# Kernel tuning notes

Hardware: AMD Instinct MI355X
Metric: run time of the kernel (lower is better)

The kernel has to match this reference:

```python
import jax, jax.numpy as jnp
import numpy as np

LATENT_SHAPES = [(192, 2, 2), (48, 4, 4), (24, 8, 8), (12, 16, 16), (6, 32, 32)]
B = 4          # batch
M = 32         # num_bases
HT, WT = 32, 32  # target spatial size = spatial size of z[-1] = (H/2, W/2)
EPS = 1e-3
CT = sum(s[0] for s in LATENT_SHAPES)  # 282


def _forward_fft(zs):
    # strided zero-insertion upsample of each latent to (HT, WT), concat channels, 2D FFT
    ups = []
    for zi in zs:
        b, c, h, w = zi.shape
        rh, rw = HT // h, WT // w
        u = jnp.zeros((b, c, HT, WT), zi.dtype).at[..., ::rh, ::rw].set(zi)
        ups.append(u)
    z = jnp.concatenate(ups, axis=1)            # (B, CT, HT, WT)
    return jnp.fft.fftn(z, axes=(-2, -1))       # complex64


def _inverse_fft(v_fft):
    # inverse FFT, take real part, split channels per level, strided downsample
    v = jnp.fft.ifftn(v_fft, axes=(-2, -1)).real  # (B, M, CT, HT, WT)
    splits = np.cumsum([s[0] for s in LATENT_SHAPES])[:-1]
    parts = jnp.split(v, splits, axis=-3)
    out = []
    for vi, (c, h, w) in zip(parts, LATENT_SHAPES):
        rh, rw = HT // h, WT // w
        out.append(vi[..., ::rh, ::rw])           # (B, M, c, h, w)
    return out


def _vector_field(zs, L, lam):
    z_fft = _forward_fft(zs)
    La = (L - jnp.swapaxes(L, -1, -2)).astype(jnp.complex64)        # antisymmetric (M, CT, CT)
    lam_a = (lam - jnp.roll(jnp.flip(lam, (1, 2)), (1, 1), axis=(1, 2))) * 1j  # (M, HT, WT) imaginary
    v_fft = jnp.einsum('mcd,bchw->bmdhw', La, z_fft)                 # (B, M, CT, HT, WT) complex
    v_fft = v_fft * lam_a[None, :, None, :, :]
    return _inverse_fft(v_fft)


def _log_prob(ws, zs, L, lam):
    S_ww = sum(jnp.einsum('bchw,bchw->b', wi, wi) for wi in ws)      # (B,)
    v = _vector_field(zs, L, lam)
    S_zz = sum(jnp.einsum('bnchw,bmchw->bnm', vi, vi) for vi in v)   # (B, M, M)
    S_zw = sum(jnp.einsum('bnchw,bchw->bn', vi, wi) for vi, wi in zip(v, ws))  # (B, M)
    var = jnp.maximum(jnp.mean(jnp.diagonal(S_zz, axis1=-2, axis2=-1), -1), 1e-6)
    std = jnp.sqrt(var)
    S_zz = S_zz / var[:, None, None]
    S_zw = S_zw / std[:, None]
    I = jnp.eye(M, dtype=S_zz.dtype)
    Mm = S_zz + EPS * I
    trace = EPS * S_ww + jnp.einsum('bn,bn->b', S_zw, S_zw)
    Lh = jnp.linalg.cholesky(Mm)
    logdet = 2.0 * jnp.sum(jnp.log(jnp.diagonal(Lh, axis1=-2, axis2=-1)), -1)
    return 0.5 * (logdet - trace)


def setup_inputs() -> dict:
    key = jax.random.key(0)
    ks = jax.random.split(key, 12)
    inp = {}
    for i, (c, h, w) in enumerate(LATENT_SHAPES):
        inp[f'z{i}'] = jax.random.normal(ks[i], (B, c, h, w), jnp.float32)
        inp[f'w{i}'] = jax.random.normal(ks[5 + i], (B, c, h, w), jnp.float32)
    inp['L'] = jax.random.normal(ks[10], (M, CT, CT), jnp.float32) * np.float32(1.0 / np.sqrt(CT))
    inp['lam'] = jax.random.normal(ks[11], (M, HT, WT), jnp.float32)
    return inp


def reference(z0, z1, z2, z3, z4, w0, w1, w2, w3, w4, L, lam):
    return _log_prob([w0, w1, w2, w3, w4], [z0, z1, z2, z3, z4], L, lam)
```

## Files before the change

kernel.cpp:

```cpp
#include <hip/hip_runtime.h>
#include <math.h>

#define NB 4
#define NM 32
#define CTOT 282
#define EPSV 1e-3f

__constant__ int g_cL[5]   = {192,48,24,12,6};
__constant__ int g_hL[5]   = {2,4,8,16,32};
__constant__ int g_coff[5] = {0,192,240,264,276};
__constant__ int g_zo[5]   = {0,768,1536,3072,6144};
__constant__ int g_po[4]   = {0,4,20,84};

__constant__ int t_lo[48] = {0,0,0,0,0,0,0,0,0,0,0,0,0,0,0,0,
                             0,0,0,0,0,0,0,0,0,0,0,0,0,0,0,0,
                             1,1,1,1,1,1,1,1, 2,2,2,2, 3,3, 4,4};
__constant__ int t_d0[48] = {0,6,12,18,24,30,36,42,48,54,60,66,72,78,84,90,
                             96,102,108,114,120,126,132,138,144,150,156,162,168,174,180,186,
                             192,198,204,210,216,222,228,234, 240,246,252,258, 264,270, 276,279};
__constant__ int t_nd[48] = {6,6,6,6,6,6,6,6,6,6,6,6,6,6,6,6,
                             6,6,6,6,6,6,6,6,6,6,6,6,6,6,6,6,
                             6,6,6,6,6,6,6,6, 6,6,6,6, 6,6, 3,3};

__constant__ int dft_l[30]  = {0,0,0, 1,1,1, 2,2,2,2,2,2,
                               3,3,3,3,3,3,3,3,3,3,3,3, 4,4,4,4,4,4};
__constant__ int dft_c0[30] = {0,64,128, 0,16,32, 0,4,8,12,16,20,
                               0,1,2,3,4,5,6,7,8,9,10,11, 0,1,2,3,4,5};
__constant__ int dft_nc[30] = {64,64,64, 16,16,16, 4,4,4,4,4,4,
                               1,1,1,1,1,1,1,1,1,1,1,1, 1,1,1,1,1,1};

#define N_LA     (NM*CTOT*CTOT)
#define OFF_LAT  0
#define OFF_ZRE  (OFF_LAT + N_LA)
#define OFF_ZIM  (OFF_ZRE + NB*12288)
#define OFF_WRE  (OFF_ZIM + NB*12288)
#define OFF_WIM  (OFF_WRE + NB*12288)
#define OFF_LAM  (OFF_WIM + NB*12288)
#define OFF_LAMF (OFF_LAM + NM*1024)
#define OFF_UR   (OFF_LAMF + NM*340)
#define OFF_UI   (OFF_UR + NB*NM*6*340)
#define OFF_VRE  (OFF_UI + NB*NM*6*340)
#define OFF_VIM  (OFF_VRE + NB*NM*12288)
#define OFF_SZZ  (OFF_VIM + NB*NM*12288)
#define OFF_SZW  (OFF_SZZ + NB*NM*NM)
#define OFF_SWW  (OFF_SZW + NB*NM)

#define PRE_LAT   (NM*81)
#define PRE_LAMF  (PRE_LAT + NM)
#define PRE_DFT   (PRE_LAMF + 2*NB*30)
#define PRE_SWW   (PRE_DFT + NB)
#define PRE_ZERO  (PRE_SWW + 17)

__global__ void __launch_bounds__(256) k_pre(
    const float* z0,const float* z1,const float* z2,const float* z3,const float* z4,
    const float* w0,const float* w1,const float* w2,const float* w3,const float* w4,
    const float* __restrict__ L, const float* __restrict__ lam, float* __restrict__ ws){
  __shared__ float shm[3136];
  int bid = blockIdx.x, t = threadIdx.x;
  if (bid < PRE_LAT){
    float* A  = shm;
    float* Bt = shm + 1056;
    int m = bid/81; int tl = bid%81;
    int d0 = (tl/9)*32, c0 = (tl%9)*32;
    const float* Lm = L + (size_t)m*CTOT*CTOT;
    for (int i=t;i<1024;i+=256){
      int r=i>>5, c=i&31;
      A[r*33+c]  = (c0+r<CTOT && d0+c<CTOT) ? Lm[(c0+r)*CTOT + d0+c] : 0.f;
      Bt[r*33+c] = (d0+r<CTOT && c0+c<CTOT) ? Lm[(d0+r)*CTOT + c0+c] : 0.f;
    }
    __syncthreads();
    float* out = ws + OFF_LAT + (size_t)m*CTOT*CTOT;
    for (int i=t;i<1024;i+=256){
      int r=i>>5, c=i&31;
      if (d0+r<CTOT && c0+c<CTOT)
        out[(size_t)(d0+r)*CTOT + c0+c] = A[c*33+r] - Bt[r*33+c];
    }
    return;
  }
  if (bid < PRE_LAMF){
    float* sA = shm;
    float* f3 = shm + 1024;
    float* f2 = shm + 1280;
    float* f1 = shm + 1344;
    int m = bid - PRE_LAT;
    for (int k=t;k<1024;k+=256){
      int ky=k>>5, kx=k&31;
      int nk = (((32-ky)&31)<<5) | ((32-kx)&31);
      float v = lam[(m<<10)+k] - lam[(m<<10)+nk];
      sA[k]=v;
      ws[OFF_LAM+(m<<10)+k]=v;
    }
    __syncthreads();
    { int s=t; int ky=s>>4, kx=s&15;
      float v = sA[(ky<<5)+kx]+sA[((ky+16)<<5)+kx]+sA[(ky<<5)+kx+16]+sA[((ky+16)<<5)+kx+16];
      f3[s]=v; ws[OFF_LAMF+m*340+84+s]=v; }
    __syncthreads();
    if (t<64){ int ky=t>>3, kx=t&7;
      float v = f3[(ky<<4)+kx]+f3[((ky+8)<<4)+kx]+f3[(ky<<4)+kx+8]+f3[((ky+8)<<4)+kx+8];
      f2[t]=v; ws[OFF_LAMF+m*340+20+t]=v; }
    __syncthreads();
    if (t<16){ int ky=t>>2, kx=t&3;
      float v = f2[(ky<<3)+kx]+f2[((ky+4)<<3)+kx]+f2[(ky<<3)+kx+4]+f2[((ky+4)<<3)+kx+4];
      f1[t]=v; ws[OFF_LAMF+m*340+4+t]=v; }
    __syncthreads();
    if (t<4){ int ky=t>>1, kx=t&1;
      float v = f1[(ky<<2)+kx]+f1[((ky+2)<<2)+kx]+f1[(ky<<2)+kx+2]+f1[((ky+2)<<2)+kx+2];
      ws[OFF_LAMF+m*340+t]=v; }
    return;
  }
  if (bid < PRE_DFT){
    float* sIn = shm;
    float* s1r = shm + 1024;
    float* s1i = shm + 2048;
    float* lc  = shm + 3072;
    float* lsn = shm + 3104;
    int i0 = bid - PRE_LAMF;
    int which = i0 / (NB*30);
    int rem = i0 % (NB*30);
    int b = rem / 30, j = rem % 30;
    int l = dft_l[j], c0 = dft_c0[j], nc = dft_nc[j];
    int h = g_hL[l], n = h*h;
    int elems = nc*n;
    const float* src;
    switch (which*5 + l){
      case 0: src=z0; break; case 1: src=z1; break; case 2: src=z2; break;
      case 3: src=z3; break; case 4: src=z4; break;
      case 5: src=w0; break; case 6: src=w1; break; case 7: src=w2; break;
      case 8: src=w3; break; default: src=w4; break;
    }
    for (int i=t;i<elems;i+=256) sIn[i] = src[(b*g_cL[l] + c0)*n + i];
    if (t<h){
      float ang = -6.2831853071795864f * (float)t / (float)h;
      lc[t] = cosf(ang); lsn[t] = sinf(ang);
    }
    __syncthreads();
    for (int p=t;p<elems;p+=256){
      int p2=p%n, cc=p/n;
      int y=p2/h, kx=p2-y*h;
      float re=0.f, im=0.f;
      for (int x=0;x<h;x++){
        int id = (kx*x)%h;
        float v = sIn[cc*n + y*h + x];
        re += v*lc[id]; im += v*lsn[id];
      }
      s1r[p]=re; s1i[p]=im;
    }
    __syncthreads();
    float scale = which ? 1.0f/(float)h : 1.0f;
    float* outR = ws + (which?OFF_WRE:OFF_ZRE) + b*12288 + g_zo[l] + c0*n;
    float* outI = ws + (which?OFF_WIM:OFF_ZIM) + b*12288 + g_zo[l] + c0*n;
    for (int p=t;p<elems;p+=256){
      int p2=p%n, cc=p/n;
      int ky=p2/h, kx=p2-(p2/h)*h;
      float re=0.f, im=0.f;
      for (int y=0;y<h;y++){
        int id=(ky*y)%h;
        float c=lc[id], s=lsn[id];
        float ar=s1r[cc*n + y*h + kx], ai=s1i[cc*n + y*h + kx];
        re += ar*c - ai*s;
        im += ar*s + ai*c;
      }
      outR[p]=re*scale; outI[p]=im*scale;
    }
    return;
  }
  if (bid < PRE_SWW){
    float* red = shm;
    int b = bid - PRE_DFT;
    const float* ptr[5] = {w0,w1,w2,w3,w4};
    float s = 0.f;
    for (int l=0;l<5;l++){
      int sz = g_cL[l]*g_hL[l]*g_hL[l];
      const float* p = ptr[l] + b*sz;
      for (int i=t;i<sz;i+=256){ float v=p[i]; s += v*v; }
    }
    red[t]=s; __syncthreads();
    for (int o=128;o>0;o>>=1){ if (t<o) red[t]+=red[t+o]; __syncthreads(); }
    if (t==0) ws[OFF_SWW + b] = red[0];
    return;
  }
  int i = (bid - PRE_SWW)*256 + t;
  if (i < NB*NM*NM + NB*NM) ws[OFF_SZZ + i] = 0.f;
}

__global__ void k_u(float* __restrict__ ws){
  __shared__ float pr[1024], pi[1024], q3r[256],q3i[256],q2r[64],q2i[64],q1r[16],q1i[16];
  int bid = blockIdx.x, t = threadIdx.x;
  int c = bid%6; int m = (bid/6)%NM; int b = bid/(6*NM);
  const float* la = ws+OFF_LAM+(m<<10);
  const float* zr = ws+OFF_ZRE+b*12288+6144+(c<<10);
  const float* zi = ws+OFF_ZIM+b*12288+6144+(c<<10);
  for (int k=t;k<1024;k+=256){ float f=la[k]; pr[k]=f*zr[k]; pi[k]=f*zi[k]; }
  __syncthreads();
  size_t base = (size_t)((b*NM+m)*6+c)*340;
  float* UR = ws+OFF_UR+base; float* UI = ws+OFF_UI+base;
  { int s=t; int ky=s>>4, kx=s&15;
    float r = pr[(ky<<5)+kx]+pr[((ky+16)<<5)+kx]+pr[(ky<<5)+kx+16]+pr[((ky+16)<<5)+kx+16];
    float ii= pi[(ky<<5)+kx]+pi[((ky+16)<<5)+kx]+pi[(ky<<5)+kx+16]+pi[((ky+16)<<5)+kx+16];
    q3r[s]=r; q3i[s]=ii; UR[84+s]=r; UI[84+s]=ii; }
  __syncthreads();
  if (t<64){ int ky=t>>3, kx=t&7;
    float r = q3r[(ky<<4)+kx]+q3r[((ky+8)<<4)+kx]+q3r[(ky<<4)+kx+8]+q3r[((ky+8)<<4)+kx+8];
    float ii= q3i[(ky<<4)+kx]+q3i[((ky+8)<<4)+kx]+q3i[(ky<<4)+kx+8]+q3i[((ky+8)<<4)+kx+8];
    q2r[t]=r; q2i[t]=ii; UR[20+t]=r; UI[20+t]=ii; }
  __syncthreads();
  if (t<16){ int ky=t>>2, kx=t&3;
    float r = q2r[(ky<<3)+kx]+q2r[((ky+4)<<3)+kx]+q2r[(ky<<3)+kx+4]+q2r[((ky+4)<<3)+kx+4];
    float ii= q2i[(ky<<3)+kx]+q2i[((ky+4)<<3)+kx]+q2i[(ky<<3)+kx+4]+q2i[((ky+4)<<3)+kx+4];
    q1r[t]=r; q1i[t]=ii; UR[4+t]=r; UI[4+t]=ii; }
  __syncthreads();
  if (t<4){ int ky=t>>1, kx=t&1;
    float r = q1r[(ky<<2)+kx]+q1r[((ky+2)<<2)+kx]+q1r[(ky<<2)+kx+2]+q1r[((ky+2)<<2)+kx+2];
    float ii= q1i[(ky<<2)+kx]+q1i[((ky+2)<<2)+kx]+q1i[(ky<<2)+kx+2]+q1i[((ky+2)<<2)+kx+2];
    UR[t]=r; UI[t]=ii; }
}

__global__ void __launch_bounds__(256) k_fold(float* __restrict__ ws){
  __shared__ float smem[9232];
  float* pre   = smem;
  float* pim   = smem + 2040;
  float* partr = smem + 4080;
  float* parti = smem + 5616;
  float* sLa   = smem + 7152;
  float* c64r  = smem + 7152;
  float* c64i  = smem + 7536;
  float* c16r  = smem + 7920;
  float* c16i  = smem + 8016;
  float* c4r   = smem + 8112;
  float* c4i   = smem + 8136;
  float* lamf  = smem + 8856;
  float* ssla  = smem + 9196;

  int t = threadIdx.x, bid = blockIdx.x;
  int m    = bid / (NB*48);
  int rem  = bid % (NB*48);
  int b    = rem / 48;
  int tile = rem % 48;
  int lo = t_lo[tile], d0 = t_d0[tile], nd = t_nd[tile];
  int ho = g_hL[lo];
  int nbins = ho*ho;
  const float* zreb = ws + OFF_ZRE + b*12288;
  const float* zimb = ws + OFF_ZIM + b*12288;
  const float* latm = ws + OFF_LAT + (size_t)m*CTOT*CTOT;

  for (int i=t;i<340;i+=256) lamf[i] = ws[OFF_LAMF + m*340 + i];
  for (int i=t;i<nd*282;i+=256){ int d=i/282, c=i-d*282; sLa[d*284+c] = latm[(size_t)(d0+d)*CTOT + c]; }
  if (t<nd*6){ int d=t/6, c=t-d*6; ssla[t] = latm[(size_t)(d0+d)*CTOT + 276 + c]; }

  int lA, kkA, c0A, nA;
  if (t<64){ lA=0; kkA=t&3; c0A=(t>>2)*12; nA=4; }
  else if (t<128){ int i=t-64; lA=1; kkA=i&15; c0A=(i>>4)*12; nA=16; }
  else { int i=t-128; lA=2; kkA=i&63; c0A=(i>>6)*12; nA=64; }
  float zAr[12], zAi[12], zBr[12], zBi[12];
  {
    const float* zr = zreb + g_zo[lA] + kkA;
    const float* zi = zimb + g_zo[lA] + kkA;
    #pragma unroll
    for (int c=0;c<12;c++){ zAr[c]=zr[(c0A+c)*nA]; zAi[c]=zi[(c0A+c)*nA]; }
    const float* zr3 = zreb + 3072 + t;
    const float* zi3 = zimb + 3072 + t;
    #pragma unroll
    for (int c=0;c<12;c++){ zBr[c]=zr3[c*256]; zBi[c]=zi3[c*256]; }
  }
  __syncthreads();

  int offA = g_coff[lA] + c0A;
  for (int d=0; d<nd; d++){
    const float4* laA = (const float4*)(sLa + d*284 + offA);
    const float4* laB = (const float4*)(sLa + d*284 + 264);
    float4 a0=laA[0], a1=laA[1], a2=laA[2];
    float4 b0=laB[0], b1=laB[1], b2=laB[2];
    float av[12] = {a0.x,a0.y,a0.z,a0.w, a1.x,a1.y,a1.z,a1.w, a2.x,a2.y,a2.z,a2.w};
    float bv[12] = {b0.x,b0.y,b0.z,b0.w, b1.x,b1.y,b1.z,b1.w, b2.x,b2.y,b2.z,b2.w};
    float prA=0.f, piA=0.f, prB=0.f, piB=0.f;
    #pragma unroll
    for (int c=0;c<12;c++){ prA+=av[c]*zAr[c]; piA+=av[c]*zAi[c]; }
    #pragma unroll
    for (int c=0;c<12;c++){ prB+=bv[c]*zBr[c]; piB+=bv[c]*zBi[c]; }
    partr[(d<<8)+t]=prA; parti[(d<<8)+t]=piA;
    pre[d*340+84+t]=prB; pim[d*340+84+t]=piB;
  }
  __syncthreads();

  for (int idx=t; idx<nd*84; idx+=256){
    int d=idx/84, s=idx-d*84;
    int base=d<<8;
    float r=0.f, ii=0.f;
    if (s<4){ for (int ch=0;ch<16;ch++){ int p=base+((ch<<2)|s); r+=partr[p]; ii+=parti[p]; } }
    else if (s<20){ int kk=s-4; for (int ch=0;ch<4;ch++){ int p=base+64+((ch<<4)|kk); r+=partr[p]; ii+=parti[p]; } }
    else { int kk=s-20; for (int ch=0;ch<2;ch++){ int p=base+128+((ch<<6)|kk); r+=partr[p]; ii+=parti[p]; } }
    pre[d*340+s]=r; pim[d*340+s]=ii;
  }
  __syncthreads();

  float sc = (float)ho/1024.f;
  if (lo==4){
    int dlb = d0 - 276;
    const float* lamA = ws + OFF_LAM + (m<<10);
    float* vRb = ws + OFF_VRE + (size_t)(b*NM+m)*12288 + 6144 + (dlb<<10);
    float* vIb = ws + OFF_VIM + (size_t)(b*NM+m)*12288 + 6144 + (dlb<<10);
    const float* z4r = zreb + 6144;
    const float* z4i = zimb + 6144;
    for (int q=t; q<1024; q+=256){
      int ky=q>>5, kx=q&31;
      int a0=((ky&1)<<1)|(kx&1);
      int a1=4+(((ky&3)<<2)|(kx&3));
      int a2=20+(((ky&7)<<3)|(kx&7));
      int a3=84+(((ky&15)<<4)|(kx&15));
      float zr_[6], zi_[6];
      #pragma unroll
      for (int c=0;c<6;c++){ zr_[c]=z4r[(c<<10)+q]; zi_[c]=z4i[(c<<10)+q]; }
      float lm = lamA[q]*sc;
      for (int d=0; d<nd; d++){
        const float* pd = pre + d*340; const float* qd = pim + d*340;
        float Br = pd[a0]+pd[a1]+pd[a2]+pd[a3];
        float Bi = qd[a0]+qd[a1]+qd[a2]+qd[a3];
        #pragma unroll
        for (int c=0;c<6;c++){ float a=ssla[d*6+c]; Br+=a*zr_[c]; Bi+=a*zi_[c]; }
        vRb[(d<<10)+q] = -lm*Bi;
        vIb[(d<<10)+q] =  lm*Br;
      }
    }
    return;
  }

  if (lo<3){
    for (int idx=t; idx<nd*64; idx+=256){
      int d=idx>>6, k2=idx&63, ky=k2>>3, kx=k2&7;
      const float* pd = pre + d*340 + 84; const float* qd = pim + d*340 + 84;
      float r=0.f, ii=0.f;
      #pragma unroll
      for (int jy=0;jy<2;jy++)
        #pragma unroll
        for (int jx=0;jx<2;jx++){
          int a = ((ky+8*jy)<<4) | (kx+8*jx);
          float f = lamf[84+a];
          r += f*pd[a]; ii += f*qd[a];
        }
      if (lo<2){ float f=lamf[20+k2]; r+=f*pre[d*340+20+k2]; ii+=f*pim[d*340+20+k2]; }
      c64r[idx]=r; c64i[idx]=ii;
    }
  }
  {
    const float* URg = ws + OFF_UR + (size_t)((b*NM+m)*6)*340 + g_po[lo];
    const float* UIg = ws + OFF_UI + (size_t)((b*NM+m)*6)*340 + g_po[lo];
    for (int idx=t; idx<6*nbins; idx+=256){
      int c=idx/nbins, bin=idx-c*nbins;
      partr[idx]=URg[c*340+bin];
      parti[idx]=UIg[c*340+bin];
    }
  }
  __syncthreads();
  if (lo<2){
    for (int idx=t; idx<nd*16; idx+=256){
      int d=idx>>4, k2=idx&15, ky=k2>>2, kx=k2&3, base=d<<6;
      float r = c64r[base+(ky<<3)+kx]+c64r[base+((ky+4)<<3)+kx]+c64r[base+(ky<<3)+kx+4]+c64r[base+((ky+4)<<3)+kx+4];
      float ii= c64i[base+(ky<<3)+kx]+c64i[base+((ky+4)<<3)+kx]+c64i[base+(ky<<3)+kx+4]+c64i[base+((ky+4)<<3)+kx+4];
      if (lo<1){ float f=lamf[4+k2]; r+=f*pre[d*340+4+k2]; ii+=f*pim[d*340+4+k2]; }
      c16r[idx]=r; c16i[idx]=ii;
    }
  }
  __syncthreads();
  if (lo==0 && t<nd*4){
    int d=t>>2, k2=t&3, ky=k2>>1, kx=k2&1, base=d<<4;
    c4r[t]=c16r[base+(ky<<2)+kx]+c16r[base+((ky+2)<<2)+kx]+c16r[base+(ky<<2)+kx+2]+c16r[base+((ky+2)<<2)+kx+2];
    c4i[t]=c16i[base+(ky<<2)+kx]+c16i[base+((ky+2)<<2)+kx]+c16i[base+(ky<<2)+kx+2]+c16i[base+((ky+2)<<2)+kx+2];
  }
  __syncthreads();

  int dlb = d0 - g_coff[lo];
  float* vRb = ws + OFF_VRE + (size_t)(b*NM+m)*12288 + g_zo[lo];
  float* vIb = ws + OFF_VIM + (size_t)(b*NM+m)*12288 + g_zo[lo];
  for (int idx=t; idx<nd*nbins; idx+=256){
    int d=idx/nbins, bin=idx-d*nbins;
    int ky=bin/ho, kx=bin-ky*ho;
    const float* pd = pre + d*340; const float* qd = pim + d*340;
    float Br = pd[((ky&1)<<1)|(kx&1)], Bi = qd[((ky&1)<<1)|(kx&1)];
    if (lo>=1){ int ix=4+(((ky&3)<<2)|(kx&3)); Br+=pd[ix]; Bi+=qd[ix]; }
    if (lo>=2){ int ix=20+(((ky&7)<<3)|(kx&7)); Br+=pd[ix]; Bi+=qd[ix]; }
    if (lo>=3){ int ix=84+(((ky&15)<<4)|(kx&15)); Br+=pd[ix]; Bi+=qd[ix]; }
    float lf = lamf[g_po[lo]+bin];
    float Vr = lf*Br, Vi = lf*Bi;
    if (lo==2){ Vr+=c64r[(d<<6)+bin]; Vi+=c64i[(d<<6)+bin]; }
    else if (lo==1){ Vr+=c16r[(d<<4)+bin]; Vi+=c16i[(d<<4)+bin]; }
    else if (lo==0){ Vr+=c4r[(d<<2)+bin]; Vi+=c4i[(d<<2)+bin]; }
    #pragma unroll
    for (int c=0;c<6;c++){ float a=ssla[d*6+c]; Vr+=a*partr[c*nbins+bin]; Vi+=a*parti[c*nbins+bin]; }
    int ob = (dlb+d)*nbins + bin;
    vRb[ob] = -sc*Vi;
    vIb[ob] =  sc*Vr;
  }
}

__global__ void __launch_bounds__(256) k_gram(float* __restrict__ ws){
  __shared__ float tile[32*260];
  __shared__ float wv[256];
  int t = threadIdx.x;
  int bid = blockIdx.x;
  int b = bid / 96, ch = bid % 96;
  int half = ch / 48;
  int k0 = (ch % 48) * 256;
  const float* V = ws + (half?OFF_VIM:OFF_VRE);
  const float* W = ws + (half?OFF_WIM:OFF_WRE) + b*12288 + k0;
  for (int i=t;i<32*256;i+=256){
    int r=i>>8, c=i&255;
    tile[r*260+c] = V[(size_t)(b*NM+r)*12288 + k0 + c];
  }
  wv[t] = W[t];
  __syncthreads();
  const float4* tf = (const float4*)tile;
  int n0 = t>>5, mm = t&31;
  float acc0=0.f, acc1=0.f, acc2=0.f, acc3=0.f;
  const float4* rm = tf + mm*65;
  const float4* r0 = tf + n0*65;
  const float4* r1 = tf + (n0+8)*65;
  const float4* r2 = tf + (n0+16)*65;
  const float4* r3 = tf + (n0+24)*65;
  for (int k4=0;k4<64;k4++){
    float4 vm = rm[k4];
    float4 v0 = r0[k4];
    float4 v1 = r1[k4];
    float4 v2 = r2[k4];
    float4 v3 = r3[k4];
    acc0 += v0.x*vm.x + v0.y*vm.y + v0.z*vm.z + v0.w*vm.w;
    acc1 += v1.x*vm.x + v1.y*vm.y + v1.z*vm.z + v1.w*vm.w;
    acc2 += v2.x*vm.x + v2.y*vm.y + v2.z*vm.z + v2.w*vm.w;
    acc3 += v3.x*vm.x + v3.y*vm.y + v3.z*vm.z + v3.w*vm.w;
  }
  float* szz = ws + OFF_SZZ + (b<<10);
  atomicAdd(&szz[(n0<<5) + mm], acc0);
  atomicAdd(&szz[((n0+8)<<5) + mm], acc1);
  atomicAdd(&szz[((n0+16)<<5) + mm], acc2);
  atomicAdd(&szz[((n0+24)<<5) + mm], acc3);
  if (t < 32){
    const float4* rn = tf + t*65;
    const float4* wf = (const float4*)wv;
    float acc=0.f;
    for (int k4=0;k4<64;k4++){
      float4 a = rn[k4]; float4 wq = wf[k4];
      acc += a.x*wq.x + a.y*wq.y + a.z*wq.z + a.w*wq.w;
    }
    atomicAdd(&ws[OFF_SZW + (b<<5) + t], acc);
  }
}

__global__ void k_final(float* __restrict__ ws, float* __restrict__ out){
  __shared__ float A[32][33];
  __shared__ float svar;
  int b = blockIdx.x, t = threadIdx.x;
  const float* szz = ws + OFF_SZZ + (b<<10);
  if (t==0){
    float s=0.f;
    for (int i=0;i<32;i++) s += szz[i*33];
    svar = fmaxf(s/32.0f, 1e-6f);
  }
  __syncthreads();
  float var = svar;
  for (int i=t;i<1024;i+=64){
    int r=i>>5, c=i&31;
    A[r][c] = szz[i]/var + ((r==c)?EPSV:0.0f);
  }
  __syncthreads();
  for (int j=0;j<32;j++){
    if (t==0) A[j][j] = sqrtf(A[j][j]);
    __syncthreads();
    if (t>j && t<32) A[t][j] /= A[j][j];
    __syncthreads();
    if (t>j && t<32){
      float lij = A[t][j];
      for (int k=j+1;k<=t;k++) A[t][k] -= lij*A[k][j];
    }
    __syncthreads();
  }
  if (t==0){
    float logdet=0.f;
    for (int j=0;j<32;j++) logdet += logf(A[j][j]);
    logdet *= 2.0f;
    const float* szw = ws + OFF_SZW + (b<<5);
    float s2=0.f;
    for (int n=0;n<32;n++) s2 += szw[n]*szw[n];
    float trace = EPSV*ws[OFF_SWW + b] + s2/var;
    out[b] = 0.5f*(logdet - trace);
  }
}

extern "C" void kernel_launch(void* const* d_in, const int* in_sizes, int n_in,
                              void* d_out, int out_size, void* d_ws, size_t ws_size,
                              hipStream_t stream){
  const float* z0 = (const float*)d_in[0];
  const float* w0 = (const float*)d_in[1];
  const float* z1 = (const float*)d_in[2];
  const float* w1 = (const float*)d_in[3];
  const float* z2 = (const float*)d_in[4];
  const float* w2 = (const float*)d_in[5];
  const float* z3 = (const float*)d_in[6];
  const float* w3 = (const float*)d_in[7];
  const float* z4 = (const float*)d_in[8];
  const float* w4 = (const float*)d_in[9];
  const float* L   = (const float*)d_in[10];
  const float* lam = (const float*)d_in[11];
  float* ws = (float*)d_ws;
  float* out = (float*)d_out;

  k_pre<<<PRE_ZERO, 256, 0, stream>>>(z0,z1,z2,z3,z4,w0,w1,w2,w3,w4, L, lam, ws);
  k_u<<<NB*NM*6, 256, 0, stream>>>(ws);
  k_fold<<<NB*NM*48, 256, 0, stream>>>(ws);
  k_gram<<<NB*96, 256, 0, stream>>>(ws);
  k_final<<<NB, 64, 0, stream>>>(ws, out);
}
```

Baseline: 213.3 us.

## Fuse final Cholesky into gram kernel and shrink fold shared memory

The final per-batch Cholesky/log-prob kernel is folded into k_gram. The last block to finish, detected through an atomic counter and threadfence, does the Cholesky for all four batches at once, one wavefront per batch. In k_fold, the per-bin partial channel sums are reduced with wavefront shuffles instead of a shared-memory pass and an extra barrier. The U staging into shared memory is removed in favour of direct global reads, which cuts shared memory from about 36KB to about 24KB so more blocks can be resident. The costs are a last-block serial tail, uncoalesced global reads in the inner loop, and a dependence on the counter being reset each launch.

```diff
diff --git a/kernel.cpp b/kernel.cpp
--- a/kernel.cpp
+++ b/kernel.cpp
@@ -44,6 +44,9 @@
 #define OFF_SZZ  (OFF_VIM + NB*NM*12288)
 #define OFF_SZW  (OFF_SZZ + NB*NM*NM)
 #define OFF_SWW  (OFF_SZW + NB*NM)
+#define OFF_CNT  (OFF_SWW + NB)
+
+#define GRAM_BLOCKS (NB*96)
 
 #define PRE_LAT   (NM*81)
 #define PRE_LAMF  (PRE_LAT + NM)
@@ -179,6 +182,7 @@
     if (t==0) ws[OFF_SWW + b] = red[0];
     return;
   }
+  if (bid == PRE_SWW && t == 0) ((unsigned*)(ws + OFF_CNT))[0] = 0u;
   int i = (bid - PRE_SWW)*256 + t;
   if (i < NB*NM*NM + NB*NM) ws[OFF_SZZ + i] = 0.f;
 }
@@ -216,20 +220,18 @@
 }
 
 __global__ void __launch_bounds__(256) k_fold(float* __restrict__ ws){
-  __shared__ float smem[9232];
+  __shared__ float smem[6160];
   float* pre   = smem;
   float* pim   = smem + 2040;
-  float* partr = smem + 4080;
-  float* parti = smem + 5616;
-  float* sLa   = smem + 7152;
-  float* c64r  = smem + 7152;
-  float* c64i  = smem + 7536;
-  float* c16r  = smem + 7920;
-  float* c16i  = smem + 8016;
-  float* c4r   = smem + 8112;
-  float* c4i   = smem + 8136;
-  float* lamf  = smem + 8856;
-  float* ssla  = smem + 9196;
+  float* sLa   = smem + 4080;
+  float* c64r  = smem + 4080;
+  float* c64i  = smem + 4464;
+  float* c16r  = smem + 4848;
+  float* c16i  = smem + 4944;
+  float* c4r   = smem + 5040;
+  float* c4i   = smem + 5064;
+  float* lamf  = smem + 5784;
+  float* ssla  = smem + 6124;
 
   int t = threadIdx.x, bid = blockIdx.x;
   int m    = bid / (NB*48);
@@ -247,10 +249,10 @@
   for (int i=t;i<nd*282;i+=256){ int d=i/282, c=i-d*282; sLa[d*284+c] = latm[(size_t)(d0+d)*CTOT + c]; }
   if (t<nd*6){ int d=t/6, c=t-d*6; ssla[t] = latm[(size_t)(d0+d)*CTOT + 276 + c]; }
 
-  int lA, kkA, c0A, nA;
-  if (t<64){ lA=0; kkA=t&3; c0A=(t>>2)*12; nA=4; }
-  else if (t<128){ int i=t-64; lA=1; kkA=i&15; c0A=(i>>4)*12; nA=16; }
-  else { int i=t-128; lA=2; kkA=i&63; c0A=(i>>6)*12; nA=64; }
+  int lA, kkA, c0A, nA, offP; bool wrt;
+  if (t<64){ lA=0; kkA=t&3; c0A=(t>>2)*12; nA=4; offP=0; wrt=(t<4); }
+  else if (t<128){ int i=t-64; lA=1; kkA=i&15; c0A=(i>>4)*12; nA=16; offP=4; wrt=(i<16); }
+  else { int i=t-128; lA=2; kkA=i>>1; c0A=(i&1)*12; nA=64; offP=20; wrt=((i&1)==0); }
   float zAr[12], zAi[12], zBr[12], zBi[12];
   {
     const float* zr = zreb + g_zo[lA] + kkA;
@@ -277,19 +279,19 @@
     for (int c=0;c<12;c++){ prA+=av[c]*zAr[c]; piA+=av[c]*zAi[c]; }
     #pragma unroll
     for (int c=0;c<12;c++){ prB+=bv[c]*zBr[c]; piB+=bv[c]*zBi[c]; }
-    partr[(d<<8)+t]=prA; parti[(d<<8)+t]=piA;
+    if (t<64){
+      prA += __shfl_xor(prA, 4);  piA += __shfl_xor(piA, 4);
+      prA += __shfl_xor(prA, 8);  piA += __shfl_xor(piA, 8);
+      prA += __shfl_xor(prA,16);  piA += __shfl_xor(piA,16);
+      prA += __shfl_xor(prA,32);  piA += __shfl_xor(piA,32);
+    } else if (t<128){
+      prA += __shfl_xor(prA,16);  piA += __shfl_xor(piA,16);
+      prA += __shfl_xor(prA,32);  piA += __shfl_xor(piA,32);
+    } else {
+      prA += __shfl_xor(prA, 1);  piA += __shfl_xor(piA, 1);
+    }
+    if (wrt){ pre[d*340+offP+kkA]=prA; pim[d*340+offP+kkA]=piA; }
     pre[d*340+84+t]=prB; pim[d*340+84+t]=piB;
-  }
-  __syncthreads();
-
-  for (int idx=t; idx<nd*84; idx+=256){
-    int d=idx/84, s=idx-d*84;
-    int base=d<<8;
-    float r=0.f, ii=0.f;
-    if (s<4){ for (int ch=0;ch<16;ch++){ int p=base+((ch<<2)|s); r+=partr[p]; ii+=parti[p]; } }
-    else if (s<20){ int kk=s-4; for (int ch=0;ch<4;ch++){ int p=base+64+((ch<<4)|kk); r+=partr[p]; ii+=parti[p]; } }
-    else { int kk=s-20; for (int ch=0;ch<2;ch++){ int p=base+128+((ch<<6)|kk); r+=partr[p]; ii+=parti[p]; } }
-    pre[d*340+s]=r; pim[d*340+s]=ii;
   }
   __syncthreads();
 
@@ -341,15 +343,6 @@
       c64r[idx]=r; c64i[idx]=ii;
     }
   }
-  {
-    const float* URg = ws + OFF_UR + (size_t)((b*NM+m)*6)*340 + g_po[lo];
-    const float* UIg = ws + OFF_UI + (size_t)((b*NM+m)*6)*340 + g_po[lo];
-    for (int idx=t; idx<6*nbins; idx+=256){
-      int c=idx/nbins, bin=idx-c*nbins;
-      partr[idx]=URg[c*340+bin];
-      parti[idx]=UIg[c*340+bin];
-    }
-  }
   __syncthreads();
   if (lo<2){
     for (int idx=t; idx<nd*16; idx+=256){
@@ -371,6 +364,8 @@
   int dlb = d0 - g_coff[lo];
   float* vRb = ws + OFF_VRE + (size_t)(b*NM+m)*12288 + g_zo[lo];
   float* vIb = ws + OFF_VIM + (size_t)(b*NM+m)*12288 + g_zo[lo];
+  const float* URg = ws + OFF_UR + (size_t)((b*NM+m)*6)*340 + g_po[lo];
+  const float* UIg = ws + OFF_UI + (size_t)((b*NM+m)*6)*340 + g_po[lo];
   for (int idx=t; idx<nd*nbins; idx+=256){
     int d=idx/nbins, bin=idx-d*nbins;
     int ky=bin/ho, kx=bin-ky*ho;
@@ -385,16 +380,17 @@
     else if (lo==1){ Vr+=c16r[(d<<4)+bin]; Vi+=c16i[(d<<4)+bin]; }
     else if (lo==0){ Vr+=c4r[(d<<2)+bin]; Vi+=c4i[(d<<2)+bin]; }
     #pragma unroll
-    for (int c=0;c<6;c++){ float a=ssla[d*6+c]; Vr+=a*partr[c*nbins+bin]; Vi+=a*parti[c*nbins+bin]; }
+    for (int c=0;c<6;c++){ float a=ssla[d*6+c]; Vr+=a*URg[c*340+bin]; Vi+=a*UIg[c*340+bin]; }
     int ob = (dlb+d)*nbins + bin;
     vRb[ob] = -sc*Vi;
     vIb[ob] =  sc*Vr;
   }
 }
 
-__global__ void __launch_bounds__(256) k_gram(float* __restrict__ ws){
+__global__ void __launch_bounds__(256) k_gram(float* __restrict__ ws, float* __restrict__ out){
   __shared__ float tile[32*260];
   __shared__ float wv[256];
+  __shared__ unsigned sdone;
   int t = threadIdx.x;
   int bid = blockIdx.x;
   int b = bid / 96, ch = bid % 96;
@@ -442,45 +438,47 @@
     }
     atomicAdd(&ws[OFF_SZW + (b<<5) + t], acc);
   }
-}
-
-__global__ void k_final(float* __restrict__ ws, float* __restrict__ out){
-  __shared__ float A[32][33];
-  __shared__ float svar;
-  int b = blockIdx.x, t = threadIdx.x;
-  const float* szz = ws + OFF_SZZ + (b<<10);
-  if (t==0){
-    float s=0.f;
-    for (int i=0;i<32;i++) s += szz[i*33];
-    svar = fmaxf(s/32.0f, 1e-6f);
-  }
-  __syncthreads();
-  float var = svar;
-  for (int i=t;i<1024;i+=64){
+  __threadfence();
+  if (t==0) sdone = atomicAdd((unsigned*)(ws + OFF_CNT), 1u);
+  __syncthreads();
+  if (sdone != GRAM_BLOCKS-1) return;
+
+  volatile const float* szzv = ws + OFF_SZZ;
+  volatile const float* szwv = ws + OFF_SZW;
+  float* A = tile;
+  int bb = t>>6, tt = t&63;
+  float* Ab = A + bb*1056;
+  float v = (tt<32) ? szzv[(bb<<10) + tt*33] : 0.f;
+  v += __shfl_xor(v,1); v += __shfl_xor(v,2); v += __shfl_xor(v,4);
+  v += __shfl_xor(v,8); v += __shfl_xor(v,16);
+  float var = fmaxf(__shfl(v,0) / 32.0f, 1e-6f);
+  for (int i=tt;i<1024;i+=64){
     int r=i>>5, c=i&31;
-    A[r][c] = szz[i]/var + ((r==c)?EPSV:0.0f);
+    Ab[r*33+c] = szzv[(bb<<10)+i]/var + ((r==c)?EPSV:0.0f);
   }
   __syncthreads();
   for (int j=0;j<32;j++){
-    if (t==0) A[j][j] = sqrtf(A[j][j]);
-    __syncthreads();
-    if (t>j && t<32) A[t][j] /= A[j][j];
-    __syncthreads();
-    if (t>j && t<32){
-      float lij = A[t][j];
-      for (int k=j+1;k<=t;k++) A[t][k] -= lij*A[k][j];
-    }
-    __syncthreads();
-  }
-  if (t==0){
-    float logdet=0.f;
-    for (int j=0;j<32;j++) logdet += logf(A[j][j]);
-    logdet *= 2.0f;
-    const float* szw = ws + OFF_SZW + (b<<5);
-    float s2=0.f;
-    for (int n=0;n<32;n++) s2 += szw[n]*szw[n];
-    float trace = EPSV*ws[OFF_SWW + b] + s2/var;
-    out[b] = 0.5f*(logdet - trace);
+    if (tt==0) Ab[j*33+j] = sqrtf(Ab[j*33+j]);
+    __syncthreads();
+    if (tt>j && tt<32) Ab[tt*33+j] /= Ab[j*33+j];
+    __syncthreads();
+    if (tt>j && tt<32){
+      float lij = Ab[tt*33+j];
+      for (int k=j+1;k<=tt;k++) Ab[tt*33+k] -= lij*Ab[k*33+j];
+    }
+    __syncthreads();
+  }
+  float ld = (tt<32) ? logf(Ab[tt*33+tt]) : 0.f;
+  ld += __shfl_xor(ld,1); ld += __shfl_xor(ld,2); ld += __shfl_xor(ld,4);
+  ld += __shfl_xor(ld,8); ld += __shfl_xor(ld,16);
+  float s2 = 0.f;
+  if (tt<32){ float x = szwv[(bb<<5)+tt]; s2 = x*x; }
+  s2 += __shfl_xor(s2,1); s2 += __shfl_xor(s2,2); s2 += __shfl_xor(s2,4);
+  s2 += __shfl_xor(s2,8); s2 += __shfl_xor(s2,16);
+  if (tt==0){
+    float logdet = 2.0f*ld;
+    float trace = EPSV*ws[OFF_SWW + bb] + s2/var;
+    out[bb] = 0.5f*(logdet - trace);
   }
 }
 
@@ -505,6 +503,5 @@
   k_pre<<<PRE_ZERO, 256, 0, stream>>>(z0,z1,z2,z3,z4,w0,w1,w2,w3,w4, L, lam, ws);
   k_u<<<NB*NM*6, 256, 0, stream>>>(ws);
   k_fold<<<NB*NM*48, 256, 0, stream>>>(ws);
-  k_gram<<<NB*96, 256, 0, stream>>>(ws);
-  k_final<<<NB, 64, 0, stream>>>(ws, out);
+  k_gram<<<GRAM_BLOCKS, 256, 0, stream>>>(ws, out);
 }
```

Result: slower. 233.5 us (+9.5%).

## Replace partial-sum LDS reduction with wave shuffles and shrink k_fold/k_gram shared memory

Applied to the files above, without the earlier changes.

In k_fold, the per-thread partial dot products for the low levels are now reduced with cross-lane xor shuffles instead of being written to shared scratch and summed in a separate pass. This removes one barrier and the partr/parti buffers. The U-term staging in shared memory is dropped in favour of direct global reads, cutting k_fold shared memory from about 37KB to 25KB to allow more resident blocks. k_gram is split into twice as many blocks with half-width tiles and float4 global loads, raising parallelism at the cost of twice as many atomic adds. The thread-to-element mapping for level 2 is also changed so the shuffle pairs line up.

```diff
diff --git a/kernel.cpp b/kernel.cpp
--- a/kernel.cpp
+++ b/kernel.cpp
@@ -216,20 +216,18 @@
 }
 
 __global__ void __launch_bounds__(256) k_fold(float* __restrict__ ws){
-  __shared__ float smem[9232];
+  __shared__ float smem[6160];
   float* pre   = smem;
   float* pim   = smem + 2040;
-  float* partr = smem + 4080;
-  float* parti = smem + 5616;
-  float* sLa   = smem + 7152;
-  float* c64r  = smem + 7152;
-  float* c64i  = smem + 7536;
-  float* c16r  = smem + 7920;
-  float* c16i  = smem + 8016;
-  float* c4r   = smem + 8112;
-  float* c4i   = smem + 8136;
-  float* lamf  = smem + 8856;
-  float* ssla  = smem + 9196;
+  float* sLa   = smem + 4080;
+  float* c64r  = smem + 4080;
+  float* c64i  = smem + 4464;
+  float* c16r  = smem + 4848;
+  float* c16i  = smem + 4944;
+  float* c4r   = smem + 5040;
+  float* c4i   = smem + 5064;
+  float* lamf  = smem + 5784;
+  float* ssla  = smem + 6124;
 
   int t = threadIdx.x, bid = blockIdx.x;
   int m    = bid / (NB*48);
@@ -247,10 +245,10 @@
   for (int i=t;i<nd*282;i+=256){ int d=i/282, c=i-d*282; sLa[d*284+c] = latm[(size_t)(d0+d)*CTOT + c]; }
   if (t<nd*6){ int d=t/6, c=t-d*6; ssla[t] = latm[(size_t)(d0+d)*CTOT + 276 + c]; }
 
-  int lA, kkA, c0A, nA;
-  if (t<64){ lA=0; kkA=t&3; c0A=(t>>2)*12; nA=4; }
-  else if (t<128){ int i=t-64; lA=1; kkA=i&15; c0A=(i>>4)*12; nA=16; }
-  else { int i=t-128; lA=2; kkA=i&63; c0A=(i>>6)*12; nA=64; }
+  int lA, kkA, c0A, nA, offP; bool wrt;
+  if (t<64){ lA=0; kkA=t&3; c0A=(t>>2)*12; nA=4; offP=0; wrt=(t<4); }
+  else if (t<128){ int i=t-64; lA=1; kkA=i&15; c0A=(i>>4)*12; nA=16; offP=4; wrt=(i<16); }
+  else { int i=t-128; lA=2; kkA=i>>1; c0A=(i&1)*12; nA=64; offP=20; wrt=((i&1)==0); }
   float zAr[12], zAi[12], zBr[12], zBi[12];
   {
     const float* zr = zreb + g_zo[lA] + kkA;
@@ -277,19 +275,19 @@
     for (int c=0;c<12;c++){ prA+=av[c]*zAr[c]; piA+=av[c]*zAi[c]; }
     #pragma unroll
     for (int c=0;c<12;c++){ prB+=bv[c]*zBr[c]; piB+=bv[c]*zBi[c]; }
-    partr[(d<<8)+t]=prA; parti[(d<<8)+t]=piA;
+    if (t<64){
+      prA += __shfl_xor(prA, 4);  piA += __shfl_xor(piA, 4);
+      prA += __shfl_xor(prA, 8);  piA += __shfl_xor(piA, 8);
+      prA += __shfl_xor(prA,16);  piA += __shfl_xor(piA,16);
+      prA += __shfl_xor(prA,32);  piA += __shfl_xor(piA,32);
+    } else if (t<128){
+      prA += __shfl_xor(prA,16);  piA += __shfl_xor(piA,16);
+      prA += __shfl_xor(prA,32);  piA += __shfl_xor(piA,32);
+    } else {
+      prA += __shfl_xor(prA, 1);  piA += __shfl_xor(piA, 1);
+    }
+    if (wrt){ pre[d*340+offP+kkA]=prA; pim[d*340+offP+kkA]=piA; }
     pre[d*340+84+t]=prB; pim[d*340+84+t]=piB;
-  }
-  __syncthreads();
-
-  for (int idx=t; idx<nd*84; idx+=256){
-    int d=idx/84, s=idx-d*84;
-    int base=d<<8;
-    float r=0.f, ii=0.f;
-    if (s<4){ for (int ch=0;ch<16;ch++){ int p=base+((ch<<2)|s); r+=partr[p]; ii+=parti[p]; } }
-    else if (s<20){ int kk=s-4; for (int ch=0;ch<4;ch++){ int p=base+64+((ch<<4)|kk); r+=partr[p]; ii+=parti[p]; } }
-    else { int kk=s-20; for (int ch=0;ch<2;ch++){ int p=base+128+((ch<<6)|kk); r+=partr[p]; ii+=parti[p]; } }
-    pre[d*340+s]=r; pim[d*340+s]=ii;
   }
   __syncthreads();
 
@@ -341,15 +339,6 @@
       c64r[idx]=r; c64i[idx]=ii;
     }
   }
-  {
-    const float* URg = ws + OFF_UR + (size_t)((b*NM+m)*6)*340 + g_po[lo];
-    const float* UIg = ws + OFF_UI + (size_t)((b*NM+m)*6)*340 + g_po[lo];
-    for (int idx=t; idx<6*nbins; idx+=256){
-      int c=idx/nbins, bin=idx-c*nbins;
-      partr[idx]=URg[c*340+bin];
-      parti[idx]=UIg[c*340+bin];
-    }
-  }
   __syncthreads();
   if (lo<2){
     for (int idx=t; idx<nd*16; idx+=256){
@@ -371,6 +360,8 @@
   int dlb = d0 - g_coff[lo];
   float* vRb = ws + OFF_VRE + (size_t)(b*NM+m)*12288 + g_zo[lo];
   float* vIb = ws + OFF_VIM + (size_t)(b*NM+m)*12288 + g_zo[lo];
+  const float* URg = ws + OFF_UR + (size_t)((b*NM+m)*6)*340 + g_po[lo];
+  const float* UIg = ws + OFF_UI + (size_t)((b*NM+m)*6)*340 + g_po[lo];
   for (int idx=t; idx<nd*nbins; idx+=256){
     int d=idx/nbins, bin=idx-d*nbins;
     int ky=bin/ho, kx=bin-ky*ho;
@@ -385,7 +376,7 @@
     else if (lo==1){ Vr+=c16r[(d<<4)+bin]; Vi+=c16i[(d<<4)+bin]; }
     else if (lo==0){ Vr+=c4r[(d<<2)+bin]; Vi+=c4i[(d<<2)+bin]; }
     #pragma unroll
-    for (int c=0;c<6;c++){ float a=ssla[d*6+c]; Vr+=a*partr[c*nbins+bin]; Vi+=a*parti[c*nbins+bin]; }
+    for (int c=0;c<6;c++){ float a=ssla[d*6+c]; Vr+=a*URg[c*340+bin]; Vi+=a*UIg[c*340+bin]; }
     int ob = (dlb+d)*nbins + bin;
     vRb[ob] = -sc*Vi;
     vIb[ob] =  sc*Vr;
@@ -393,30 +384,33 @@
 }
 
 __global__ void __launch_bounds__(256) k_gram(float* __restrict__ ws){
-  __shared__ float tile[32*260];
-  __shared__ float wv[256];
+  __shared__ float tile[32*132];
+  __shared__ float wv[128];
   int t = threadIdx.x;
   int bid = blockIdx.x;
-  int b = bid / 96, ch = bid % 96;
-  int half = ch / 48;
-  int k0 = (ch % 48) * 256;
+  int b = bid / 192, ch = bid % 192;
+  int half = ch / 96;
+  int k0 = (ch % 96) * 128;
   const float* V = ws + (half?OFF_VIM:OFF_VRE);
   const float* W = ws + (half?OFF_WIM:OFF_WRE) + b*12288 + k0;
-  for (int i=t;i<32*256;i+=256){
-    int r=i>>8, c=i&255;
-    tile[r*260+c] = V[(size_t)(b*NM+r)*12288 + k0 + c];
-  }
-  wv[t] = W[t];
+  #pragma unroll
+  for (int p=0;p<4;p++){
+    int i4 = t + (p<<8);
+    int row = i4 >> 5, c4 = i4 & 31;
+    float4 v = *(const float4*)(V + (size_t)(b*NM+row)*12288 + k0 + (c4<<2));
+    *(float4*)(tile + row*132 + (c4<<2)) = v;
+  }
+  if (t<128) wv[t] = W[t];
   __syncthreads();
   const float4* tf = (const float4*)tile;
   int n0 = t>>5, mm = t&31;
   float acc0=0.f, acc1=0.f, acc2=0.f, acc3=0.f;
-  const float4* rm = tf + mm*65;
-  const float4* r0 = tf + n0*65;
-  const float4* r1 = tf + (n0+8)*65;
-  const float4* r2 = tf + (n0+16)*65;
-  const float4* r3 = tf + (n0+24)*65;
-  for (int k4=0;k4<64;k4++){
+  const float4* rm = tf + mm*33;
+  const float4* r0 = tf + n0*33;
+  const float4* r1 = tf + (n0+8)*33;
+  const float4* r2 = tf + (n0+16)*33;
+  const float4* r3 = tf + (n0+24)*33;
+  for (int k4=0;k4<32;k4++){
     float4 vm = rm[k4];
     float4 v0 = r0[k4];
     float4 v1 = r1[k4];
@@ -433,10 +427,10 @@
   atomicAdd(&szz[((n0+16)<<5) + mm], acc2);
   atomicAdd(&szz[((n0+24)<<5) + mm], acc3);
   if (t < 32){
-    const float4* rn = tf + t*65;
+    const float4* rn = tf + t*33;
     const float4* wf = (const float4*)wv;
     float acc=0.f;
-    for (int k4=0;k4<64;k4++){
+    for (int k4=0;k4<32;k4++){
       float4 a = rn[k4]; float4 wq = wf[k4];
       acc += a.x*wq.x + a.y*wq.y + a.z*wq.z + a.w*wq.w;
     }
@@ -505,6 +499,6 @@
   k_pre<<<PRE_ZERO, 256, 0, stream>>>(z0,z1,z2,z3,z4,w0,w1,w2,w3,w4, L, lam, ws);
   k_u<<<NB*NM*6, 256, 0, stream>>>(ws);
   k_fold<<<NB*NM*48, 256, 0, stream>>>(ws);
-  k_gram<<<NB*96, 256, 0, stream>>>(ws);
+  k_gram<<<NB*192, 256, 0, stream>>>(ws);
   k_final<<<NB, 64, 0, stream>>>(ws, out);
 }
```

Result: faster. 206.0 us (-3.4%).
